# Kernel optimization log

Measured on AMD Instinct MI355X. Metric: run time of the kernel, lower is better.

Reference implementation:

```python
import jax, jax.numpy as jnp
import numpy as np

B, L, D, N, KEEP, HID = 64, 256, 128, 8192, 64, 1024
IN_DIM = D + KEEP * D + 1  # q + packed subset keys + log_count


def setup_inputs() -> dict:
    key = jax.random.key(0)
    ks = jax.random.split(key, 7)
    q = jax.random.normal(ks[0], (N, D), jnp.float32)
    k = jax.random.normal(ks[1], (B, L, D), jnp.float32)
    batch_idx = jax.random.randint(ks[2], (N,), 0, B)
    mask = jax.random.randint(ks[3], (N, L), 0, 2).astype(bool)
    count = jax.random.randint(ks[4], (N,), 0, L)
    W1 = jax.random.normal(ks[5], (IN_DIM, HID), jnp.float32) / np.sqrt(IN_DIM).astype(np.float32)
    b1 = jnp.zeros((HID,), jnp.float32)
    W2 = jax.random.normal(ks[6], (HID, 1), jnp.float32) / np.sqrt(HID).astype(np.float32)
    b2 = jnp.zeros((1,), jnp.float32)
    return dict(q=q, k=k, batch_idx=batch_idx, mask=mask, count=count,
                W1=W1, b1=b1, W2=W2, b2=b2)


def _pack_subset_keys(k, batch_idx, mask):
    # chain_k: [N, L, D] gather of per-chain key blocks
    chain_k = k[batch_idx]
    pos = jnp.arange(L, dtype=jnp.float32)
    # score = L - pos for masked positions, 0 otherwise -> topk picks first KEEP masked positions
    scores = mask.astype(jnp.float32) * (jnp.float32(L) - pos)[None, :]
    top_scores, top_idx = jax.lax.top_k(scores, KEEP)
    picked = top_scores > 0
    sortable = jnp.where(picked, top_idx, L)  # sentinel L for unpicked
    sortable = jnp.sort(sortable, axis=1)     # restore ascending position order
    picked = sortable < L
    safe_idx = jnp.where(picked, sortable, 0)
    packed = jnp.take_along_axis(chain_k, safe_idx[:, :, None], axis=1)  # [N, KEEP, D]
    packed = packed * picked[:, :, None].astype(packed.dtype)
    return packed.reshape(N, KEEP * D)


def reference(q, k, batch_idx, mask, count, W1, b1, W2, b2):
    packed = _pack_subset_keys(k, batch_idx, mask)
    log_count = jnp.log1p(count.astype(q.dtype))[:, None]
    feat = jnp.concatenate([q, packed, log_count], axis=-1)  # [N, IN_DIM]
    h = jax.nn.gelu(feat @ W1 + b1, approximate=False)       # torch GELU = exact erf
    return (h @ W2 + b2).squeeze(-1)                          # [N]
```

## Files before the change

kernel.cpp:

```cpp
#include <hip/hip_runtime.h>
#include <math.h>

#define N_ROWS 8192
#define B_CH   64
#define L_SEQ  256
#define D_DIM  128
#define KEEP   64
#define HID    1024
#define KTOT   8320

#define KOFF   (N_ROWS * D_DIM)
#define ZOFF   (KOFF + B_CH * L_SEQ * D_DIM)
#define BUF_ELEMS (ZOFF + 128)

#define PACK_BLOCKS 256
#define QK_BLOCKS   1537
#define W1T_BLOCKS  2080
#define OUT_BLOCKS  32
#define PREP_GRID   (PACK_BLOCKS + QK_BLOCKS + W1T_BLOCKS + OUT_BLOCKS)

typedef unsigned short ushort_t;
typedef __attribute__((ext_vector_type(8))) short  short8;
typedef __attribute__((ext_vector_type(4))) float  float4v;

__device__ __forceinline__ ushort_t f2bf(float f) {
    union { float f; unsigned int u; } v; v.f = f;
    unsigned int u = v.u;
    unsigned int r = u + 0x7fffu + ((u >> 16) & 1u);
    return (ushort_t)(r >> 16);
}

__device__ __forceinline__ void glds16(const void* g, void* l) {
    __builtin_amdgcn_global_load_lds(
        (const __attribute__((address_space(1))) unsigned int*)g,
        (__attribute__((address_space(3))) unsigned int*)l,
        16, 0, 0);
}

__global__ void prep(const float* __restrict__ q, const float* __restrict__ k,
                     const float* __restrict__ W1, const int* __restrict__ mask,
                     const int* __restrict__ batch_idx, const int* __restrict__ count,
                     const float* __restrict__ b2,
                     ushort_t* __restrict__ buf, ushort_t* __restrict__ w1t,
                     int* __restrict__ srcLUT, float* __restrict__ logc,
                     float* __restrict__ out) {
    __shared__ __align__(16) char smem[16640];
    const int blk = blockIdx.x;
    const int t = threadIdx.x;

    if (blk < PACK_BLOCKS) {
        const int n0 = blk * 32;
        int* sidx = (int*)smem;
        int* bidx_l = (int*)(smem + 32 * 65 * 4);
        for (int i = t; i < 32 * 65; i += 256) sidx[i] = -1;
        if (t < 32) {
            int n = n0 + t;
            bidx_l[t] = batch_idx[n];
            logc[n] = log1pf((float)count[n]);
            srcLUT[n] = n * D_DIM;
        }
        __syncthreads();
        const int w = t >> 6, l = t & 63;
        const unsigned long long ltm = (1ull << l) - 1ull;
        for (int r = 0; r < 8; ++r) {
            const int lr = w * 8 + r;
            const int* mrow = mask + (size_t)(n0 + lr) * L_SEQ;
            int m0 = mrow[l] != 0;
            int m1 = mrow[64 + l] != 0;
            int m2 = mrow[128 + l] != 0;
            int m3 = mrow[192 + l] != 0;
            unsigned long long b0 = __ballot(m0), b1 = __ballot(m1);
            unsigned long long b2v = __ballot(m2), b3 = __ballot(m3);
            int p1 = (int)__popcll(b0);
            int p2 = p1 + (int)__popcll(b1);
            int p3 = p2 + (int)__popcll(b2v);
            int* row = sidx + lr * 65;
            if (m0) { int rk = (int)__popcll(b0 & ltm);       if (rk < KEEP) row[rk] = l; }
            if (m1) { int rk = p1 + (int)__popcll(b1 & ltm);  if (rk < KEEP) row[rk] = 64 + l; }
            if (m2) { int rk = p2 + (int)__popcll(b2v & ltm); if (rk < KEEP) row[rk] = 128 + l; }
            if (m3) { int rk = p3 + (int)__popcll(b3 & ltm);  if (rk < KEEP) row[rk] = 192 + l; }
        }
        __syncthreads();
        for (int e = t; e < KEEP * 32; e += 256) {
            int j = e >> 5, nl = e & 31;
            int s = sidx[nl * 65 + j];
            srcLUT[(size_t)(j + 1) * N_ROWS + n0 + nl] =
                (s >= 0) ? (KOFF + (bidx_l[nl] * L_SEQ + s) * D_DIM) : ZOFF;
        }

    } else if (blk < PACK_BLOCKS + QK_BLOCKS) {
        int c = (blk - PACK_BLOCKS) * 256 + t;
        if (c >= BUF_ELEMS / 8) return;
        int e = c * 8;
        float4 x0, x1;
        if (e < KOFF) {
            const float4* s = (const float4*)(q + e);
            x0 = s[0]; x1 = s[1];
        } else if (e < ZOFF) {
            const float4* s = (const float4*)(k + (e - KOFF));
            x0 = s[0]; x1 = s[1];
        } else {
            x0 = make_float4(0.f, 0.f, 0.f, 0.f);
            x1 = x0;
        }
        union { ushort_t s[8]; uint4 v; } o;
        o.s[0] = f2bf(x0.x); o.s[1] = f2bf(x0.y); o.s[2] = f2bf(x0.z); o.s[3] = f2bf(x0.w);
        o.s[4] = f2bf(x1.x); o.s[5] = f2bf(x1.y); o.s[6] = f2bf(x1.z); o.s[7] = f2bf(x1.w);
        *(uint4*)(buf + e) = o.v;

    } else if (blk < PACK_BLOCKS + QK_BLOCKS + W1T_BLOCKS) {
        const int idx = blk - (PACK_BLOCKS + QK_BLOCKS);
        const int k0 = (idx % 130) * 64, h0 = (idx / 130) * 64;
        float (*tile)[65] = (float(*)[65])smem;
        const int hl = t & 63, kl = t >> 6;
#pragma unroll
        for (int i = 0; i < 16; ++i) {
            int kk = kl + i * 4;
            tile[kk][hl] = W1[(size_t)(k0 + kk) * HID + h0 + hl];
        }
        __syncthreads();
#pragma unroll
        for (int i = 0; i < 2; ++i) {
            int chunk = i * 256 + t;
            int h = chunk >> 3, piece = chunk & 7;
            union { ushort_t s[8]; uint4 v; } o;
#pragma unroll
            for (int j = 0; j < 8; ++j) o.s[j] = f2bf(tile[piece * 8 + j][h]);
            *(uint4*)(w1t + (size_t)(h0 + h) * KTOT + k0 + piece * 8) = o.v;
        }

    } else {
        int i = (blk - (PACK_BLOCKS + QK_BLOCKS + W1T_BLOCKS)) * 256 + t;
        if (i < N_ROWS) out[i] = b2[0];
    }
}

__global__ __launch_bounds__(256, 2)
void gemm_mlp(const ushort_t* __restrict__ buf, const ushort_t* __restrict__ w1t,
              const int* __restrict__ srcLUT, const float* __restrict__ logc,
              const float* __restrict__ W1, const float* __restrict__ b1,
              const float* __restrict__ W2, float* __restrict__ out) {
    __shared__ ushort_t As[2][128 * 64];
    __shared__ ushort_t Bs[2][128 * 64];

    const int t = threadIdx.x;
    const int blkH = blockIdx.x, blkM = blockIdx.y;
    const int wave = t >> 6, lane = t & 63;
    const int wm = wave >> 1, wh = wave & 1;
    const int ln = lane & 15, quad = lane >> 4;

    float4v acc[4][4];
#pragma unroll
    for (int i = 0; i < 4; ++i)
#pragma unroll
        for (int j = 0; j < 4; ++j)
#pragma unroll
            for (int r = 0; r < 4; ++r) acc[i][j][r] = 0.0f;

    const int tr = t >> 3;
    const int pg = (t & 7) ^ (tr & 7);
    const ushort_t* gBp[4];
#pragma unroll
    for (int i = 0; i < 4; ++i)
        gBp[i] = w1t + (size_t)(blkH * 128 + i * 32 + tr) * KTOT + pg * 8;
    const int* lutBase = srcLUT + blkM * 128 + tr;

    int offA[4], offN[4];
#pragma unroll
    for (int i = 0; i < 4; ++i) offA[i] = lutBase[i * 32];

#pragma unroll
    for (int i = 0; i < 4; ++i) {
        glds16(buf + offA[i] + pg * 8, &As[0][(i * 256 + t) * 8]);
        glds16(gBp[i], &Bs[0][(i * 256 + t) * 8]);
    }

    int p = 0;
    for (int ch = 0; ch < 130; ++ch) {
        __syncthreads();
        const int nx = ch + 1;
        if (nx < 130) {
            const int half = nx & 1;
            const int* offs = half ? offA : offN;
            ushort_t* dA = &As[p ^ 1][0];
            ushort_t* dB = &Bs[p ^ 1][0];
#pragma unroll
            for (int i = 0; i < 4; ++i) {
                glds16(buf + offs[i] + half * 64 + pg * 8, dA + (i * 256 + t) * 8);
                glds16(gBp[i] + nx * 64, dB + (i * 256 + t) * 8);
            }
        }
        if ((ch & 1) == 0 && (ch >> 1) < 64) {
#pragma unroll
            for (int i = 0; i < 4; ++i) offN[i] = lutBase[((ch >> 1) + 1) * N_ROWS + i * 32];
        }
        const ushort_t* rA = &As[p][0];
        const ushort_t* rB = &Bs[p][0];
#pragma unroll
        for (int kk = 0; kk < 2; ++kk) {
            short8 af[4], bfr[4];
#pragma unroll
            for (int mi = 0; mi < 4; ++mi) {
                const int row = wm * 64 + mi * 16 + ln;
                const int sl = (kk * 4 + quad) ^ (ln & 7);
                af[mi] = *(const short8*)(rA + row * 64 + sl * 8);
            }
#pragma unroll
            for (int ni = 0; ni < 4; ++ni) {
                const int row = wh * 64 + ni * 16 + ln;
                const int sl = (kk * 4 + quad) ^ (ln & 7);
                bfr[ni] = *(const short8*)(rB + row * 64 + sl * 8);
            }
#pragma unroll
            for (int mi = 0; mi < 4; ++mi)
#pragma unroll
                for (int ni = 0; ni < 4; ++ni)
                    acc[mi][ni] = __builtin_amdgcn_mfma_f32_16x16x32_bf16(
                        af[mi], bfr[ni], acc[mi][ni], 0, 0, 0);
        }
        if (ch & 1) {
#pragma unroll
            for (int i = 0; i < 4; ++i) offA[i] = offN[i];
        }
        p ^= 1;
    }

    const float* w1last = W1 + (size_t)KTOT * HID;
    float w1l[4], b1v[4], w2v[4];
#pragma unroll
    for (int ni = 0; ni < 4; ++ni) {
        int h = blkH * 128 + wh * 64 + ni * 16 + ln;
        w1l[ni] = w1last[h];
        b1v[ni] = b1[h];
        w2v[ni] = W2[h];
    }
    const int nbase = blkM * 128 + wm * 64 + quad * 4;
#pragma unroll
    for (int mi = 0; mi < 4; ++mi) {
#pragma unroll
        for (int rg = 0; rg < 4; ++rg) {
            const int n = nbase + mi * 16 + rg;
            const float lc = logc[n];
            float s = 0.0f;
#pragma unroll
            for (int ni = 0; ni < 4; ++ni) {
                float pre = acc[mi][ni][rg] + lc * w1l[ni] + b1v[ni];
                float hv = 0.5f * pre * (1.0f + erff(pre * 0.70710678118654752f));
                s += hv * w2v[ni];
            }
            s += __shfl_xor(s, 1);
            s += __shfl_xor(s, 2);
            s += __shfl_xor(s, 4);
            s += __shfl_xor(s, 8);
            if (ln == 0) atomicAdd(out + n, s);
        }
    }
}

extern "C" void kernel_launch(void* const* d_in, const int* in_sizes, int n_in,
                              void* d_out, int out_size, void* d_ws, size_t ws_size,
                              hipStream_t stream) {
    const float* q     = (const float*)d_in[0];
    const float* k     = (const float*)d_in[1];
    const int*   bidx  = (const int*)d_in[2];
    const int*   mask  = (const int*)d_in[3];
    const int*   count = (const int*)d_in[4];
    const float* W1    = (const float*)d_in[5];
    const float* b1    = (const float*)d_in[6];
    const float* W2    = (const float*)d_in[7];
    const float* b2    = (const float*)d_in[8];
    float* out = (float*)d_out;

    char* ws = (char*)d_ws;
    ushort_t* buf    = (ushort_t*)(ws);
    ushort_t* w1t    = (ushort_t*)(ws + 6291712);
    int*      srcLUT = (int*)(ws + 6291712 + 17039360);
    float*    logc   = (float*)(ws + 6291712 + 17039360 + 2129920);

    prep<<<PREP_GRID, 256, 0, stream>>>(q, k, W1, mask, bidx, count, b2,
                                        buf, w1t, srcLUT, logc, out);
    gemm_mlp<<<dim3(HID / 128, N_ROWS / 128), 256, 0, stream>>>(
        buf, w1t, srcLUT, logc, W1, b1, W2, out);
}
```

Measured before the change: 255.6 us.

## Specialize waves into loader producers and MFMA consumers in GEMM kernel

Splits the four waves of each GEMM block into two producer waves that issue all async global-to-LDS copies and two consumer waves that run MFMA on a wider 64x128 tile each. The aim is to take load-issue and address work off the compute waves so it overlaps with matrix math. In exchange, only half the waves issue MFMAs, and the consumers hold twice as many accumulators, which raises register pressure and risks spills or lower occupancy.

```diff
diff --git a/kernel.cpp b/kernel.cpp
--- a/kernel.cpp
+++ b/kernel.cpp
@@ -146,113 +146,126 @@
     const int t = threadIdx.x;
     const int blkH = blockIdx.x, blkM = blockIdx.y;
     const int wave = t >> 6, lane = t & 63;
-    const int wm = wave >> 1, wh = wave & 1;
     const int ln = lane & 15, quad = lane >> 4;
 
-    float4v acc[4][4];
-#pragma unroll
-    for (int i = 0; i < 4; ++i)
-#pragma unroll
-        for (int j = 0; j < 4; ++j)
-#pragma unroll
-            for (int r = 0; r < 4; ++r) acc[i][j][r] = 0.0f;
-
-    const int tr = t >> 3;
-    const int pg = (t & 7) ^ (tr & 7);
-    const ushort_t* gBp[4];
-#pragma unroll
-    for (int i = 0; i < 4; ++i)
-        gBp[i] = w1t + (size_t)(blkH * 128 + i * 32 + tr) * KTOT + pg * 8;
-    const int* lutBase = srcLUT + blkM * 128 + tr;
-
-    int offA[4], offN[4];
-#pragma unroll
-    for (int i = 0; i < 4; ++i) offA[i] = lutBase[i * 32];
-
-#pragma unroll
-    for (int i = 0; i < 4; ++i) {
-        glds16(buf + offA[i] + pg * 8, &As[0][(i * 256 + t) * 8]);
-        glds16(gBp[i], &Bs[0][(i * 256 + t) * 8]);
-    }
-
-    int p = 0;
-    for (int ch = 0; ch < 130; ++ch) {
-        __syncthreads();
-        const int nx = ch + 1;
-        if (nx < 130) {
-            const int half = nx & 1;
-            const int* offs = half ? offA : offN;
-            ushort_t* dA = &As[p ^ 1][0];
-            ushort_t* dB = &Bs[p ^ 1][0];
-#pragma unroll
-            for (int i = 0; i < 4; ++i) {
-                glds16(buf + offs[i] + half * 64 + pg * 8, dA + (i * 256 + t) * 8);
-                glds16(gBp[i] + nx * 64, dB + (i * 256 + t) * 8);
+    if (wave >= 2) {
+        const int u = (wave - 2) * 64 + lane;
+        const int tr8 = u >> 3;
+        const int pg = (u & 7) ^ (tr8 & 7);
+        const ushort_t* gBp[8];
+#pragma unroll
+        for (int i = 0; i < 8; ++i)
+            gBp[i] = w1t + (size_t)(blkH * 128 + i * 16 + tr8) * KTOT + pg * 8;
+        const int* lut = srcLUT + blkM * 128 + tr8;
+
+        int offC[8], offP[8];
+#pragma unroll
+        for (int i = 0; i < 8; ++i) offC[i] = lut[i * 16];
+#pragma unroll
+        for (int i = 0; i < 8; ++i) {
+            glds16(buf + offC[i] + pg * 8, &As[0][i * 1024 + u * 8]);
+            glds16(gBp[i], &Bs[0][i * 1024 + u * 8]);
+        }
+#pragma unroll
+        for (int i = 0; i < 8; ++i) offP[i] = lut[N_ROWS + i * 16];
+        __syncthreads();
+
+        int p = 0;
+        for (int ch = 0; ch < 130; ++ch) {
+            const int nx = ch + 1;
+            if (nx < 130) {
+                const int half = nx & 1;
+                if (half == 0) {
+#pragma unroll
+                    for (int i = 0; i < 8; ++i) offC[i] = offP[i];
+                }
+                ushort_t* dA = &As[p ^ 1][0];
+                ushort_t* dB = &Bs[p ^ 1][0];
+#pragma unroll
+                for (int i = 0; i < 8; ++i) {
+                    glds16(buf + offC[i] + half * 64 + pg * 8, dA + i * 1024 + u * 8);
+                    glds16(gBp[i] + nx * 64, dB + i * 1024 + u * 8);
+                }
+                if (half == 0) {
+                    const int nb = (nx >> 1) + 1;
+                    if (nb < 65) {
+#pragma unroll
+                        for (int i = 0; i < 8; ++i) offP[i] = lut[nb * N_ROWS + i * 16];
+                    }
+                }
             }
-        }
-        if ((ch & 1) == 0 && (ch >> 1) < 64) {
-#pragma unroll
-            for (int i = 0; i < 4; ++i) offN[i] = lutBase[((ch >> 1) + 1) * N_ROWS + i * 32];
-        }
-        const ushort_t* rA = &As[p][0];
-        const ushort_t* rB = &Bs[p][0];
-#pragma unroll
-        for (int kk = 0; kk < 2; ++kk) {
-            short8 af[4], bfr[4];
-#pragma unroll
-            for (int mi = 0; mi < 4; ++mi) {
-                const int row = wm * 64 + mi * 16 + ln;
+            __syncthreads();
+            p ^= 1;
+        }
+    } else {
+        const int wm = wave;
+        float4v acc[4][8];
+#pragma unroll
+        for (int i = 0; i < 4; ++i)
+#pragma unroll
+            for (int j = 0; j < 8; ++j)
+#pragma unroll
+                for (int r = 0; r < 4; ++r) acc[i][j][r] = 0.0f;
+
+        __syncthreads();
+        int p = 0;
+        for (int ch = 0; ch < 130; ++ch) {
+            const ushort_t* rA = &As[p][0];
+            const ushort_t* rB = &Bs[p][0];
+#pragma unroll
+            for (int kk = 0; kk < 2; ++kk) {
                 const int sl = (kk * 4 + quad) ^ (ln & 7);
-                af[mi] = *(const short8*)(rA + row * 64 + sl * 8);
+                short8 af[4], bq[8];
+#pragma unroll
+                for (int mi = 0; mi < 4; ++mi) {
+                    const int row = wm * 64 + mi * 16 + ln;
+                    af[mi] = *(const short8*)(rA + row * 64 + sl * 8);
+                }
+#pragma unroll
+                for (int ni = 0; ni < 8; ++ni) {
+                    const int row = ni * 16 + ln;
+                    bq[ni] = *(const short8*)(rB + row * 64 + sl * 8);
+                }
+#pragma unroll
+                for (int mi = 0; mi < 4; ++mi)
+#pragma unroll
+                    for (int ni = 0; ni < 8; ++ni)
+                        acc[mi][ni] = __builtin_amdgcn_mfma_f32_16x16x32_bf16(
+                            af[mi], bq[ni], acc[mi][ni], 0, 0, 0);
             }
-#pragma unroll
-            for (int ni = 0; ni < 4; ++ni) {
-                const int row = wh * 64 + ni * 16 + ln;
-                const int sl = (kk * 4 + quad) ^ (ln & 7);
-                bfr[ni] = *(const short8*)(rB + row * 64 + sl * 8);
+            __syncthreads();
+            p ^= 1;
+        }
+
+        const float* w1last = W1 + (size_t)KTOT * HID;
+        float w1l[8], b1v[8], w2v[8];
+#pragma unroll
+        for (int ni = 0; ni < 8; ++ni) {
+            int h = blkH * 128 + ni * 16 + ln;
+            w1l[ni] = w1last[h];
+            b1v[ni] = b1[h];
+            w2v[ni] = W2[h];
+        }
+        const int nbase = blkM * 128 + wm * 64 + quad * 4;
+#pragma unroll
+        for (int mi = 0; mi < 4; ++mi) {
+#pragma unroll
+            for (int rg = 0; rg < 4; ++rg) {
+                const int n = nbase + mi * 16 + rg;
+                const float lc = logc[n];
+                float s = 0.0f;
+#pragma unroll
+                for (int ni = 0; ni < 8; ++ni) {
+                    float pre = acc[mi][ni][rg] + lc * w1l[ni] + b1v[ni];
+                    float hv = 0.5f * pre * (1.0f + erff(pre * 0.70710678118654752f));
+                    s += hv * w2v[ni];
+                }
+                s += __shfl_xor(s, 1);
+                s += __shfl_xor(s, 2);
+                s += __shfl_xor(s, 4);
+                s += __shfl_xor(s, 8);
+                if (ln == 0) atomicAdd(out + n, s);
             }
-#pragma unroll
-            for (int mi = 0; mi < 4; ++mi)
-#pragma unroll
-                for (int ni = 0; ni < 4; ++ni)
-                    acc[mi][ni] = __builtin_amdgcn_mfma_f32_16x16x32_bf16(
-                        af[mi], bfr[ni], acc[mi][ni], 0, 0, 0);
-        }
-        if (ch & 1) {
-#pragma unroll
-            for (int i = 0; i < 4; ++i) offA[i] = offN[i];
-        }
-        p ^= 1;
-    }
-
-    const float* w1last = W1 + (size_t)KTOT * HID;
-    float w1l[4], b1v[4], w2v[4];
-#pragma unroll
-    for (int ni = 0; ni < 4; ++ni) {
-        int h = blkH * 128 + wh * 64 + ni * 16 + ln;
-        w1l[ni] = w1last[h];
-        b1v[ni] = b1[h];
-        w2v[ni] = W2[h];
-    }
-    const int nbase = blkM * 128 + wm * 64 + quad * 4;
-#pragma unroll
-    for (int mi = 0; mi < 4; ++mi) {
-#pragma unroll
-        for (int rg = 0; rg < 4; ++rg) {
-            const int n = nbase + mi * 16 + rg;
-            const float lc = logc[n];
-            float s = 0.0f;
-#pragma unroll
-            for (int ni = 0; ni < 4; ++ni) {
-                float pre = acc[mi][ni][rg] + lc * w1l[ni] + b1v[ni];
-                float hv = 0.5f * pre * (1.0f + erff(pre * 0.70710678118654752f));
-                s += hv * w2v[ni];
-            }
-            s += __shfl_xor(s, 1);
-            s += __shfl_xor(s, 2);
-            s += __shfl_xor(s, 4);
-            s += __shfl_xor(s, 8);
-            if (ln == 0) atomicAdd(out + n, s);
         }
     }
 }
```

New measurement: 268.3 us. 5.0% more time.
